# Performance work log

Hardware: AMD Instinct MI355X
Metric: run time of the kernel (lower is better)

## Reference

```python
import jax, jax.numpy as jnp
import numpy as np

NEG_SLOPE = 0.2
EPS = 1e-16


def gat_conv(x, src, dst, n_nodes, W, att_src, att_dst, b):
    """PyG GATConv, heads=1. x:[N,in], W:[out,in], att_*:[out], b:[out].
    Messages flow src->dst; softmax over incoming edges of each dst node."""
    h = x @ W.T                                  # [N, out]
    a_src = h @ att_src                          # [N]
    a_dst = h @ att_dst                          # [N]
    e = jax.nn.leaky_relu(a_src[src] + a_dst[dst], NEG_SLOPE)   # [E]
    m = jax.ops.segment_max(e, dst, num_segments=n_nodes)       # [N]
    ex = jnp.exp(e - m[dst])                                    # [E]
    denom = jax.ops.segment_sum(ex, dst, num_segments=n_nodes)  # [N]
    alpha = ex / (denom[dst] + EPS)                             # [E]
    out = jax.ops.segment_sum(h[src] * alpha[:, None], dst, num_segments=n_nodes)
    return out + b


def setup_inputs() -> dict:
    key = jax.random.key(0)
    ks = jax.random.split(key, 12)
    N, E = 100000, 1280000
    d_in, d_hid, d_out = 2, 64, 2

    def glorot(k, shape):
        fan = shape[-1] + shape[0]
        s = jnp.sqrt(6.0 / fan)
        return jax.random.uniform(k, shape, jnp.float32, -s, s)

    return {
        "x": jax.random.normal(ks[0], (N, d_in), jnp.float32),
        "edge_index": jax.random.randint(ks[1], (2, E), 0, N, jnp.int64)
            if jax.config.jax_enable_x64 else
            jax.random.randint(ks[1], (2, E), 0, N, jnp.int32),
        "W1": glorot(ks[2], (d_hid, d_in)),
        "att_src1": glorot(ks[3], (d_hid,)),
        "att_dst1": glorot(ks[4], (d_hid,)),
        "b1": jnp.zeros((d_hid,), jnp.float32),
        "W2": glorot(ks[5], (d_out, d_hid)),
        "att_src2": glorot(ks[6], (d_out,)),
        "att_dst2": glorot(ks[7], (d_out,)),
        "b2": jnp.zeros((d_out,), jnp.float32),
    }


def reference(x, edge_index, W1, att_src1, att_dst1, b1, W2, att_src2, att_dst2, b2):
    n_nodes = x.shape[0]
    # add self-loops (PyG GATConv default)
    loops = jnp.arange(n_nodes, dtype=edge_index.dtype)
    src = jnp.concatenate([edge_index[0], loops])
    dst = jnp.concatenate([edge_index[1], loops])

    h = gat_conv(x, src, dst, n_nodes, W1, att_src1, att_dst1, b1)
    h = jax.nn.relu(h)
    # dropout p=0.6 is identity in eval mode
    h = gat_conv(h, src, dst, n_nodes, W2, att_src2, att_dst2, b2)
    return jax.nn.log_softmax(h, axis=1)
```

## Files before the change

kernel.cpp:

```cpp
#include <hip/hip_runtime.h>
#include <cstdint>

#define NEG_SLOPE 0.2f
#define EPS 1e-16f
#define BSH 7
#define BNODES (1 << BSH)
#define NBMAX 1024
#define CAP 2560
#define EPT 32
#define MAXDEG 64
#define ROWP 65

__device__ __forceinline__ float lrelu(float x) {
    return (x >= 0.f) ? x : NEG_SLOPE * x;
}

template <int CTRL>
__device__ __forceinline__ float dpp_ror_add(float v) {
    int r = __builtin_amdgcn_update_dpp(0, __float_as_int(v), CTRL, 0xf, 0xf, true);
    return v + __int_as_float(r);
}
__device__ __forceinline__ float wave_sum(float v) {
    v = dpp_ror_add<0x121>(v);
    v = dpp_ror_add<0x122>(v);
    v = dpp_ror_add<0x124>(v);
    v = dpp_ror_add<0x128>(v);
    v += __shfl_xor(v, 16);
    v += __shfl_xor(v, 32);
    return v;
}

__global__ __launch_bounds__(1024)
void const_kernel(const float* __restrict__ W1,
                  const float* __restrict__ as1,
                  const float* __restrict__ ad1,
                  float4* __restrict__ consts,
                  int* __restrict__ gcur) {
    int tid = threadIdx.x;
    gcur[tid] = 0;
    if (tid < 64) {
        float w0 = W1[2 * tid], w1 = W1[2 * tid + 1];
        float s = as1[tid], d = ad1[tid];
        float c0 = wave_sum(w0 * s);
        float c1 = wave_sum(w1 * s);
        float e0 = wave_sum(w0 * d);
        float e1 = wave_sum(w1 * d);
        if (tid == 0) *consts = make_float4(c0, c1, e0, e1);
    }
}

__global__ __launch_bounds__(256)
void bucket_kernel(const int* __restrict__ src, const int* __restrict__ dst,
                   int* __restrict__ gcur, unsigned* __restrict__ bkt,
                   int E, int Etot, int nbuck) {
    __shared__ int cnt[NBMAX];
    __shared__ int base[NBMAX];
    int tid = threadIdx.x;
    int blockBase = blockIdx.x * (256 * EPT);
    for (int b = tid; b < nbuck; b += 256) cnt[b] = 0;
    __syncthreads();

    #pragma unroll
    for (int k = 0; k < EPT; ++k) {
        int i = blockBase + k * 256 + tid;
        if (i < Etot) {
            int d = (i < E) ? dst[i] : (i - E);
            atomicAdd(&cnt[d >> BSH], 1);
        }
    }
    __syncthreads();
    for (int b = tid; b < nbuck; b += 256) {
        int c = cnt[b];
        base[b] = c ? atomicAdd(gcur + b, c) : 0;
    }
    __syncthreads();
    for (int b = tid; b < nbuck; b += 256) cnt[b] = 0;
    __syncthreads();

    #pragma unroll
    for (int k = 0; k < EPT; ++k) {
        int i = blockBase + k * 256 + tid;
        if (i < Etot) {
            int s, d;
            if (i < E) { s = src[i]; d = dst[i]; } else { s = d = i - E; }
            int b = d >> BSH;
            unsigned p = ((unsigned)s << BSH) | (unsigned)(d & (BNODES - 1));
            int pos = base[b] + atomicAdd(&cnt[b], 1);
            if (pos < CAP) bkt[(size_t)b * CAP + pos] = p;
        }
    }
}

__global__ __launch_bounds__(128)
void agg1t_kernel(const int* __restrict__ gcur, const unsigned* __restrict__ bkt,
                  const float2* __restrict__ x, const float4* __restrict__ consts,
                  const float* __restrict__ W1, const float* __restrict__ b1,
                  const float* __restrict__ W2, const float* __restrict__ as2,
                  const float* __restrict__ ad2, float4* __restrict__ pack2,
                  int N) {
    __shared__ int rows[BNODES * ROWP];
    __shared__ int cur[BNODES];
    __shared__ float4 tab[64];
    __shared__ float w2bL[64];
    int b = blockIdx.x, tid = threadIdx.x;
    int nodeBase = b << BSH;
    cur[tid] = 0;
    if (tid < 64) {
        tab[tid] = make_float4(W1[2 * tid], W1[2 * tid + 1], b1[tid], W2[tid]);
        w2bL[tid] = W2[64 + tid];
    }
    __syncthreads();

    int cnt = gcur[b];
    if (cnt > CAP) cnt = CAP;
    const unsigned* bp = bkt + (size_t)b * CAP;
    for (int k = tid; k < cnt; k += 128) {
        unsigned p = bp[k];
        int ld = p & (BNODES - 1);
        int r = atomicAdd(&cur[ld], 1);
        if (r < MAXDEG) rows[ld * ROWP + r] = (int)(p >> BSH);
    }
    __syncthreads();

    int i = tid;
    int n = nodeBase + i;
    if (n >= N) return;
    int dg = cur[i];
    if (dg > MAXDEG) dg = MAXDEG;
    float4 c = *consts;
    float2 xn = x[n];
    float adst_n = fmaf(xn.x, c.z, xn.y * c.w);

    float sp = 0.f, s0 = 0.f, s1 = 0.f;
    for (int r = 0; r < dg; ++r) {
        int s = rows[i * ROWP + r];
        float2 xs = x[s];
        float e = lrelu(fmaf(xs.x, c.x, xs.y * c.y) + adst_n);
        float pv = __expf(e);
        sp += pv;
        s0 = fmaf(pv, xs.x, s0);
        s1 = fmaf(pv, xs.y, s1);
    }
    float rden = 1.f / (sp + EPS);
    s0 *= rden;
    s1 *= rden;

    float q0 = 0.f, q1 = 0.f;
    #pragma unroll 8
    for (int j = 0; j < 64; ++j) {
        float4 t = tab[j];
        float hr = fmaxf(fmaf(t.x, s0, t.y * s1) + t.z, 0.f);
        q0 = fmaf(hr, t.w, q0);
        q1 = fmaf(hr, w2bL[j], q1);
    }
    float sa = as2[0], sb = as2[1], da = ad2[0], db = ad2[1];
    pack2[n] = make_float4(q0, q1,
                           fmaf(q0, sa, q1 * sb),
                           fmaf(q0, da, q1 * db));
}

__global__ __launch_bounds__(128)
void agg2t_kernel(const int* __restrict__ gcur, const unsigned* __restrict__ bkt,
                  const float4* __restrict__ pack2, const float* __restrict__ b2,
                  float2* __restrict__ out, int N) {
    __shared__ int rows[BNODES * ROWP];
    __shared__ int cur[BNODES];
    int b = blockIdx.x, tid = threadIdx.x;
    int nodeBase = b << BSH;
    cur[tid] = 0;
    __syncthreads();

    int cnt = gcur[b];
    if (cnt > CAP) cnt = CAP;
    const unsigned* bp = bkt + (size_t)b * CAP;
    for (int k = tid; k < cnt; k += 128) {
        unsigned p = bp[k];
        int ld = p & (BNODES - 1);
        int r = atomicAdd(&cur[ld], 1);
        if (r < MAXDEG) rows[ld * ROWP + r] = (int)(p >> BSH);
    }
    __syncthreads();

    int i = tid;
    int n = nodeBase + i;
    if (n >= N) return;
    int dg = cur[i];
    if (dg > MAXDEG) dg = MAXDEG;
    float adst_n = ((const float*)(pack2 + n))[3];

    float sp = 0.f, a0 = 0.f, a1 = 0.f;
    for (int r = 0; r < dg; ++r) {
        int s = rows[i * ROWP + r];
        float4 P = pack2[s];
        float pv = __expf(lrelu(P.z + adst_n));
        sp += pv;
        a0 = fmaf(pv, P.x, a0);
        a1 = fmaf(pv, P.y, a1);
    }
    float rd = 1.f / (sp + EPS);
    float v0 = fmaf(a0, rd, b2[0]);
    float v1 = fmaf(a1, rd, b2[1]);
    float mx = fmaxf(v0, v1);
    float lse = mx + logf(__expf(v0 - mx) + __expf(v1 - mx));
    out[n] = make_float2(v0 - lse, v1 - lse);
}

extern "C" void kernel_launch(void* const* d_in, const int* in_sizes, int n_in,
                              void* d_out, int out_size, void* d_ws, size_t ws_size,
                              hipStream_t stream) {
    const float* x      = (const float*)d_in[0];
    const int*   eidx   = (const int*)d_in[1];
    const float* W1     = (const float*)d_in[2];
    const float* att_s1 = (const float*)d_in[3];
    const float* att_d1 = (const float*)d_in[4];
    const float* b1     = (const float*)d_in[5];
    const float* W2     = (const float*)d_in[6];
    const float* att_s2 = (const float*)d_in[7];
    const float* att_d2 = (const float*)d_in[8];
    const float* b2     = (const float*)d_in[9];

    const int N     = in_sizes[0] / 2;
    const int E     = in_sizes[1] / 2;
    const int Etot  = E + N;
    const int nbuck = (N + BNODES - 1) >> BSH;

    const int* src = eidx;
    const int* dst = eidx + E;

    char* w = (char*)(((uintptr_t)d_ws + 15) & ~(uintptr_t)15);
    int*      gcur   = (int*)w;      w += (size_t)NBMAX * 4;
    unsigned* bkt    = (unsigned*)w; w += (size_t)nbuck * CAP * 4;
    float4*   pack2  = (float4*)w;   w += (size_t)N * 16;
    float4*   consts = (float4*)w;   w += 16;

    const_kernel<<<dim3(1), dim3(1024), 0, stream>>>(W1, att_s1, att_d1, consts, gcur);

    int nblocks = (Etot + 256 * EPT - 1) / (256 * EPT);
    bucket_kernel<<<dim3(nblocks), dim3(256), 0, stream>>>(src, dst, gcur, bkt, E, Etot, nbuck);

    agg1t_kernel<<<dim3(nbuck), dim3(128), 0, stream>>>(
        gcur, bkt, (const float2*)x, consts, W1, b1, W2, att_s2, att_d2, pack2, N);

    agg2t_kernel<<<dim3(nbuck), dim3(128), 0, stream>>>(
        gcur, bkt, pack2, b2, (float2*)d_out, N);
}
```

Before: 65.54 us.

## Stage bucket payloads in LDS and shrink per-block edge chunk

The bucketing kernel now reads each edge's src/dst from global memory only once, staging the packed payload and bucket id in shared memory for the scatter pass instead of re-reading them. Blocks grow to 1024 threads handling 4 edges each (4096 edges per block instead of 8192), which roughly doubles the block count and the number of per-block global atomics on bucket cursors. The trade is fewer global reads and more parallelism against extra LDS use, more block-level atomic reservations, and scatter writes spread across more, smaller per-block runs.

```diff
diff --git a/kernel.cpp b/kernel.cpp
--- a/kernel.cpp
+++ b/kernel.cpp
@@ -7,9 +7,10 @@
 #define BNODES (1 << BSH)
 #define NBMAX 1024
 #define CAP 2560
-#define EPT 32
 #define MAXDEG 64
 #define ROWP 65
+#define BKT_T 1024
+#define BEPT 4
 
 __device__ __forceinline__ float lrelu(float x) {
     return (x >= 0.f) ? x : NEG_SLOPE * x;
@@ -49,42 +50,51 @@
     }
 }
 
-__global__ __launch_bounds__(256)
+__global__ __launch_bounds__(BKT_T)
 void bucket_kernel(const int* __restrict__ src, const int* __restrict__ dst,
                    int* __restrict__ gcur, unsigned* __restrict__ bkt,
                    int E, int Etot, int nbuck) {
     __shared__ int cnt[NBMAX];
     __shared__ int base[NBMAX];
+    __shared__ unsigned pay[BKT_T * BEPT];
+    __shared__ unsigned short pbk[BKT_T * BEPT];
     int tid = threadIdx.x;
-    int blockBase = blockIdx.x * (256 * EPT);
-    for (int b = tid; b < nbuck; b += 256) cnt[b] = 0;
+    int blockBase = blockIdx.x * (BKT_T * BEPT);
+    for (int b = tid; b < nbuck; b += BKT_T) cnt[b] = 0;
     __syncthreads();
 
     #pragma unroll
-    for (int k = 0; k < EPT; ++k) {
-        int i = blockBase + k * 256 + tid;
-        if (i < Etot) {
-            int d = (i < E) ? dst[i] : (i - E);
-            atomicAdd(&cnt[d >> BSH], 1);
+    for (int k = 0; k < BEPT; ++k) {
+        int idx = k * BKT_T + tid;
+        int i = blockBase + idx;
+        unsigned p = 0;
+        int b = 0;
+        bool ok = (i < Etot);
+        if (ok) {
+            int s, d;
+            if (i < E) { s = src[i]; d = dst[i]; } else { s = d = i - E; }
+            b = d >> BSH;
+            p = ((unsigned)s << BSH) | (unsigned)(d & (BNODES - 1));
+            atomicAdd(&cnt[b], 1);
         }
-    }
-    __syncthreads();
-    for (int b = tid; b < nbuck; b += 256) {
+        pay[idx] = ok ? p : 0xFFFFFFFFu;
+        pbk[idx] = (unsigned short)b;
+    }
+    __syncthreads();
+    for (int b = tid; b < nbuck; b += BKT_T) {
         int c = cnt[b];
         base[b] = c ? atomicAdd(gcur + b, c) : 0;
     }
     __syncthreads();
-    for (int b = tid; b < nbuck; b += 256) cnt[b] = 0;
+    for (int b = tid; b < nbuck; b += BKT_T) cnt[b] = 0;
     __syncthreads();
 
     #pragma unroll
-    for (int k = 0; k < EPT; ++k) {
-        int i = blockBase + k * 256 + tid;
-        if (i < Etot) {
-            int s, d;
-            if (i < E) { s = src[i]; d = dst[i]; } else { s = d = i - E; }
-            int b = d >> BSH;
-            unsigned p = ((unsigned)s << BSH) | (unsigned)(d & (BNODES - 1));
+    for (int k = 0; k < BEPT; ++k) {
+        int idx = k * BKT_T + tid;
+        unsigned p = pay[idx];
+        if (p != 0xFFFFFFFFu) {
+            int b = pbk[idx];
             int pos = base[b] + atomicAdd(&cnt[b], 1);
             if (pos < CAP) bkt[(size_t)b * CAP + pos] = p;
         }
@@ -235,8 +245,8 @@
 
     const_kernel<<<dim3(1), dim3(1024), 0, stream>>>(W1, att_s1, att_d1, consts, gcur);
 
-    int nblocks = (Etot + 256 * EPT - 1) / (256 * EPT);
-    bucket_kernel<<<dim3(nblocks), dim3(256), 0, stream>>>(src, dst, gcur, bkt, E, Etot, nbuck);
+    int nblocks = (Etot + BKT_T * BEPT - 1) / (BKT_T * BEPT);
+    bucket_kernel<<<dim3(nblocks), dim3(BKT_T), 0, stream>>>(src, dst, gcur, bkt, E, Etot, nbuck);
 
     agg1t_kernel<<<dim3(nbuck), dim3(128), 0, stream>>>(
         gcur, bkt, (const float2*)x, consts, W1, b1, W2, att_s2, att_d2, pack2, N);
```

Result: faster. 56.00 us (-14.6%).

## Handle self-loops analytically in aggregation and reshape bucketing launch

Applied to the files above, without the earlier changes.

Self-loop edges are no longer written into the bucket lists. Each aggregation kernel now seeds its softmax accumulators with the node's own self-loop term, computed directly from its own features. This removes N entries from bucketing, gather and atomics. The bucket kernel also moves to 1024-thread blocks with 8 edges per thread, so each thread owns one bucket counter. That mapping assumes nbuck is at most 1024. Per-bucket capacity now holds only real edges, and MAXDEG clipping excludes the self-loop.

```diff
diff --git a/kernel.cpp b/kernel.cpp
--- a/kernel.cpp
+++ b/kernel.cpp
@@ -7,9 +7,10 @@
 #define BNODES (1 << BSH)
 #define NBMAX 1024
 #define CAP 2560
-#define EPT 32
 #define MAXDEG 64
 #define ROWP 65
+#define BKT_T 1024
+#define BEPT 8
 
 __device__ __forceinline__ float lrelu(float x) {
     return (x >= 0.f) ? x : NEG_SLOPE * x;
@@ -49,44 +50,40 @@
     }
 }
 
-__global__ __launch_bounds__(256)
+__global__ __launch_bounds__(BKT_T)
 void bucket_kernel(const int* __restrict__ src, const int* __restrict__ dst,
                    int* __restrict__ gcur, unsigned* __restrict__ bkt,
-                   int E, int Etot, int nbuck) {
+                   int E, int nbuck) {
     __shared__ int cnt[NBMAX];
     __shared__ int base[NBMAX];
     int tid = threadIdx.x;
-    int blockBase = blockIdx.x * (256 * EPT);
-    for (int b = tid; b < nbuck; b += 256) cnt[b] = 0;
+    long long blockBase = (long long)blockIdx.x * (BKT_T * BEPT);
+    cnt[tid] = 0;
     __syncthreads();
 
     #pragma unroll
-    for (int k = 0; k < EPT; ++k) {
-        int i = blockBase + k * 256 + tid;
-        if (i < Etot) {
-            int d = (i < E) ? dst[i] : (i - E);
-            atomicAdd(&cnt[d >> BSH], 1);
-        }
-    }
-    __syncthreads();
-    for (int b = tid; b < nbuck; b += 256) {
-        int c = cnt[b];
-        base[b] = c ? atomicAdd(gcur + b, c) : 0;
-    }
-    __syncthreads();
-    for (int b = tid; b < nbuck; b += 256) cnt[b] = 0;
+    for (int k = 0; k < BEPT; ++k) {
+        long long i = blockBase + k * BKT_T + tid;
+        if (i < E) atomicAdd(&cnt[dst[i] >> BSH], 1);
+    }
+    __syncthreads();
+    int c = cnt[tid];
+    base[tid] = c ? atomicAdd(gcur + tid, c) : 0;
+    __syncthreads();
+    cnt[tid] = 0;
     __syncthreads();
 
     #pragma unroll
-    for (int k = 0; k < EPT; ++k) {
-        int i = blockBase + k * 256 + tid;
-        if (i < Etot) {
-            int s, d;
-            if (i < E) { s = src[i]; d = dst[i]; } else { s = d = i - E; }
-            int b = d >> BSH;
-            unsigned p = ((unsigned)s << BSH) | (unsigned)(d & (BNODES - 1));
-            int pos = base[b] + atomicAdd(&cnt[b], 1);
-            if (pos < CAP) bkt[(size_t)b * CAP + pos] = p;
+    for (int k = 0; k < BEPT; ++k) {
+        long long i = blockBase + k * BKT_T + tid;
+        if (i < E) {
+            int s = src[i], d = dst[i];
+            int bk = d >> BSH;
+            int r = atomicAdd(&cnt[bk], 1);
+            int pos = base[bk] + r;
+            if (pos < CAP)
+                bkt[(size_t)bk * CAP + pos] =
+                    ((unsigned)s << BSH) | (unsigned)(d & (BNODES - 1));
         }
     }
 }
@@ -129,9 +126,11 @@
     if (dg > MAXDEG) dg = MAXDEG;
     float4 c = *consts;
     float2 xn = x[n];
+    float asrc_n = fmaf(xn.x, c.x, xn.y * c.y);
     float adst_n = fmaf(xn.x, c.z, xn.y * c.w);
 
-    float sp = 0.f, s0 = 0.f, s1 = 0.f;
+    float pvs = __expf(lrelu(asrc_n + adst_n));
+    float sp = pvs, s0 = pvs * xn.x, s1 = pvs * xn.y;
     for (int r = 0; r < dg; ++r) {
         int s = rows[i * ROWP + r];
         float2 xs = x[s];
@@ -186,9 +185,11 @@
     if (n >= N) return;
     int dg = cur[i];
     if (dg > MAXDEG) dg = MAXDEG;
-    float adst_n = ((const float*)(pack2 + n))[3];
-
-    float sp = 0.f, a0 = 0.f, a1 = 0.f;
+    float4 Pn = pack2[n];
+    float adst_n = Pn.w;
+
+    float pvs = __expf(lrelu(Pn.z + adst_n));
+    float sp = pvs, a0 = pvs * Pn.x, a1 = pvs * Pn.y;
     for (int r = 0; r < dg; ++r) {
         int s = rows[i * ROWP + r];
         float4 P = pack2[s];
@@ -221,7 +222,6 @@
 
     const int N     = in_sizes[0] / 2;
     const int E     = in_sizes[1] / 2;
-    const int Etot  = E + N;
     const int nbuck = (N + BNODES - 1) >> BSH;
 
     const int* src = eidx;
@@ -235,8 +235,8 @@
 
     const_kernel<<<dim3(1), dim3(1024), 0, stream>>>(W1, att_s1, att_d1, consts, gcur);
 
-    int nblocks = (Etot + 256 * EPT - 1) / (256 * EPT);
-    bucket_kernel<<<dim3(nblocks), dim3(256), 0, stream>>>(src, dst, gcur, bkt, E, Etot, nbuck);
+    int nblocks = (E + BKT_T * BEPT - 1) / (BKT_T * BEPT);
+    bucket_kernel<<<dim3(nblocks), dim3(BKT_T), 0, stream>>>(src, dst, gcur, bkt, E, nbuck);
 
     agg1t_kernel<<<dim3(nbuck), dim3(128), 0, stream>>>(
         gcur, bkt, (const float2*)x, consts, W1, b1, W2, att_s2, att_d2, pack2, N);
```

Measured after the change: 53.77 us (median of 2 runs). -18.0%, faster.
